# Performance work log

Measured on AMD Instinct MI355X. Metric: run time of the kernel, lower is better.

## Reference

```python
import jax, jax.numpy as jnp
import numpy as np

B, C_IN, N_PTS = 16, 4, 4096
N_P, DIM = 32, 256
EPS = 1e-5


def conv1d(x, w, b):
    # 1x1 Conv1d: x (B,C,N), w (O,C), b (O)
    return jnp.einsum('bcn,oc->bon', x, w) + b[None, :, None]


def bn(x, g, be):
    # BatchNorm1d in training mode: batch statistics over (B, N)
    m = jnp.mean(x, axis=(0, 2), keepdims=True)
    v = jnp.var(x, axis=(0, 2), keepdims=True)
    return g[None, :, None] * (x - m) * jax.lax.rsqrt(v + EPS) + be[None, :, None]


def softpool(x, n_p=N_P):
    # x: (B, C, N). For each sorting channel c, take indices of its top n_p
    # points and gather ALL C feature channels at those points.
    _, idx = jax.lax.top_k(x, n_p)            # (B, C_sort, n_p) indices into N
    g = jax.vmap(lambda xb, ib: xb[:, ib])(x, idx)  # (B, C_feat, C_sort, n_p)
    return jnp.transpose(g, (0, 1, 3, 2))     # (B, C_feat, n_p, C_sort)


def _forward(x, w1, b1, g1, be1, w2, b2, g2, be2, w3, b3, g3, be3,
             w8, b8, w9, b9, w4, b4, g4, be4, w5, b5, g5, be5,
             w6, b6, g6, be6, w7, b7):
    h = jax.nn.relu(bn(conv1d(x, w1, b1), g1, be1))      # (B,64,N)
    pointfeat = h
    h = jax.nn.relu(bn(conv1d(h, w2, b2), g2, be2))      # (B,128,N)
    h = bn(conv1d(h, w3, b3), g3, be3)                   # (B,256,N)
    sp = softpool(h)                                     # (B,256,32,256)
    # conv8: Conv2d(256,256,(1,256)) -> (B,256,32)
    y = jnp.einsum('bchw,ocw->boh', sp, w8) + b8[None, :, None]
    # conv9: Conv2d(256,256,(32,1)) -> (B,256)
    y = jnp.einsum('bch,och->bo', y, w9) + b9[None, :]
    glob = jnp.broadcast_to(y[:, :, None], (x.shape[0], DIM, x.shape[2]))
    h = jnp.concatenate([glob, pointfeat], axis=1)       # (B,320,N)
    h = jax.nn.relu(bn(conv1d(h, w4, b4), g4, be4))      # (B,512,N)
    h = jax.nn.relu(bn(conv1d(h, w5, b5), g5, be5))      # (B,256,N)
    h = jax.nn.relu(bn(conv1d(h, w6, b6), g6, be6))      # (B,128,N)
    return jnp.tanh(conv1d(h, w7, b7))                   # (B,3,N)


def setup_inputs() -> dict:
    key = jax.random.key(0)
    ks = iter(jax.random.split(key, 64))
    def p(shape, scale=0.05):
        return (jax.random.normal(next(ks), shape, jnp.float32) * scale)
    inp = {}
    inp['x'] = jax.random.normal(next(ks), (B, C_IN, N_PTS), jnp.float32)
    for name, o, i in [('1', 64, 4), ('2', 128, 64), ('3', 256, 128),
                       ('4', 512, 320), ('5', 256, 512), ('6', 128, 256)]:
        inp['w' + name] = p((o, i))
        inp['b' + name] = p((o,))
        inp['g' + name] = jnp.ones((o,), jnp.float32)
        inp['be' + name] = jnp.zeros((o,), jnp.float32)
    inp['w7'] = p((3, 128)); inp['b7'] = p((3,))
    inp['w8'] = p((DIM, DIM, DIM)); inp['b8'] = p((DIM,))
    inp['w9'] = p((DIM, DIM, N_P)); inp['b9'] = p((DIM,))
    return inp


def reference(x, w1, b1, g1, be1, w2, b2, g2, be2, w3, b3, g3, be3,
              w4, b4, g4, be4, w5, b5, g5, be5, w6, b6, g6, be6,
              w7, b7, w8, b8, w9, b9):
    return _forward(x, w1, b1, g1, be1, w2, b2, g2, be2, w3, b3, g3, be3,
                    w8, b8, w9, b9, w4, b4, g4, be4, w5, b5, g5, be5,
                    w6, b6, g6, be6, w7, b7)
```

## Files before the change

### kernel.cpp

```cpp
#include <hip/hip_runtime.h>
#include <cstdint>
#include <cstddef>

#define NPTS 4096
#define BATCH 16

typedef unsigned int uint32;
typedef unsigned short u16;

typedef __attribute__((ext_vector_type(8))) short short8;
typedef __attribute__((ext_vector_type(16))) float float16;

__device__ __forceinline__ u16 f2bf(float f) {
  uint32 u = __float_as_uint(f);
  u = (u + 0x7fffu + ((u >> 16) & 1u)) >> 16;
  return (u16)u;
}
__device__ __forceinline__ float bf2f(u16 h) {
  return __uint_as_float(((uint32)h) << 16);
}

__global__ __launch_bounds__(256) void conv_gemm(
    const float* __restrict__ act, const float* __restrict__ wt,
    const float* __restrict__ rowbias, const float* __restrict__ obias,
    const float* __restrict__ inScale, const float* __restrict__ inShift,
    float* __restrict__ out, float* __restrict__ partials, int C, int O)
{
  __shared__ float As[16][68];
  __shared__ float Ws[16][68];
  __shared__ float redS[64][17];
  __shared__ float redQ[64][17];
  const int b  = blockIdx.z;
  const int o0 = blockIdx.y * 64;
  const int n0 = blockIdx.x * 64;
  const int t  = threadIdx.x;
  const int tx = t & 15, ty = t >> 4;
  float acc[4][4] = {};
  const float* actb = act + ((size_t)b * C) * NPTS;

  for (int k0 = 0; k0 < C; k0 += 16) {
    const int r  = ty;
    const int cs = tx * 4;
    const int k  = k0 + r;
    float4 av = make_float4(0.f, 0.f, 0.f, 0.f);
    if (k < C) {
      av = *(const float4*)(actb + (size_t)k * NPTS + n0 + cs);
      if (inScale) {
        const float scv = inScale[k], shv = inShift[k];
        av.x = fmaxf(fmaf(av.x, scv, shv), 0.f);
        av.y = fmaxf(fmaf(av.y, scv, shv), 0.f);
        av.z = fmaxf(fmaf(av.z, scv, shv), 0.f);
        av.w = fmaxf(fmaf(av.w, scv, shv), 0.f);
      }
    }
    *(float4*)&As[r][cs] = av;

    float4 wv = make_float4(0.f, 0.f, 0.f, 0.f);
    if (k < C) {
      const float* wp = wt + (size_t)k * O;
      const int o = o0 + cs;
      if (o + 3 < O) {
        wv = *(const float4*)&wp[o];
      } else {
        float tmp[4] = {0.f, 0.f, 0.f, 0.f};
        for (int j = 0; j < 4; ++j) if (o + j < O) tmp[j] = wp[o + j];
        wv = make_float4(tmp[0], tmp[1], tmp[2], tmp[3]);
      }
    }
    *(float4*)&Ws[r][cs] = wv;
    __syncthreads();

    const int kmax = (C - k0 < 16) ? (C - k0) : 16;
    for (int kk = 0; kk < kmax; ++kk) {
      float4 a = *(float4*)&As[kk][tx * 4];
      float4 w = *(float4*)&Ws[kk][ty * 4];
      acc[0][0] += w.x * a.x; acc[0][1] += w.x * a.y; acc[0][2] += w.x * a.z; acc[0][3] += w.x * a.w;
      acc[1][0] += w.y * a.x; acc[1][1] += w.y * a.y; acc[1][2] += w.y * a.z; acc[1][3] += w.y * a.w;
      acc[2][0] += w.z * a.x; acc[2][1] += w.z * a.y; acc[2][2] += w.z * a.z; acc[2][3] += w.z * a.w;
      acc[3][0] += w.w * a.x; acc[3][1] += w.w * a.y; acc[3][2] += w.w * a.z; acc[3][3] += w.w * a.w;
    }
    __syncthreads();
  }

  float s[4], q[4];
  for (int i = 0; i < 4; ++i) {
    const int o = o0 + ty * 4 + i;
    s[i] = 0.f; q[i] = 0.f;
    if (o >= O) continue;
    float base = 0.f;
    if (rowbias) base  = rowbias[(size_t)b * O + o];
    if (obias)   base += obias[o];
    float4 v = make_float4(acc[i][0] + base, acc[i][1] + base, acc[i][2] + base, acc[i][3] + base);
    *(float4*)&out[((size_t)b * O + o) * NPTS + n0 + tx * 4] = v;
    s[i] = v.x + v.y + v.z + v.w;
    q[i] = v.x * v.x + v.y * v.y + v.z * v.z + v.w * v.w;
  }

  if (partials) {
    for (int i = 0; i < 4; ++i) { redS[ty * 4 + i][tx] = s[i]; redQ[ty * 4 + i][tx] = q[i]; }
    __syncthreads();
    if (t < 64) {
      float a = 0.f;
      for (int j = 0; j < 16; ++j) a += redS[t][j];
      partials[((size_t)b * O + o0 + t) * 64 + blockIdx.x] = a;
    } else if (t < 128) {
      float a = 0.f;
      for (int j = 0; j < 16; ++j) a += redQ[t - 64][j];
      partials[(size_t)BATCH * O * 64 + ((size_t)b * O + o0 + t - 64) * 64 + blockIdx.x] = a;
    }
  }
}

__global__ __launch_bounds__(256) void pack_wmfma(const float* __restrict__ src,
                                                  u16* __restrict__ ph, u16* __restrict__ pl,
                                                  int O, int Ctot, int cOff, int Csub) {
  int i = blockIdx.x * 256 + threadIdx.x;
  if (i >= O * Csub) return;
  const int KS = Csub >> 4;
  int j    = i & 7;
  int lj   = (i >> 3) & 63;
  int mtks = i >> 9;
  int ks   = mtks % KS;
  int mt   = mtks / KS;
  int o = mt * 32 + (lj & 31);
  int c = ks * 16 + (lj >> 5) * 8 + j;
  float v = src[(size_t)o * Ctot + cOff + c];
  u16 h = f2bf(v);
  ph[i] = h;
  pl[i] = f2bf(v - bf2f(h));
}

__global__ __launch_bounds__(256) void conv_mfma(
    const float* __restrict__ act, const u16* __restrict__ wh, const u16* __restrict__ wl,
    const float* __restrict__ rowbias,
    const float* __restrict__ inScale, const float* __restrict__ inShift,
    float* __restrict__ out, float* __restrict__ ps, int C, int O)
{
  __shared__ u16 Bh[4096];
  __shared__ u16 Bl[4096];
  const int b  = blockIdx.z;
  const int o0 = blockIdx.y * 128;
  const int n0 = blockIdx.x * 128;
  const int t  = threadIdx.x;
  const int l  = t & 63, wva = t >> 6;
  const int mt = blockIdx.y * 4 + wva;
  const int KS = C >> 4;
  const float* actb = act + ((size_t)b * C) * NPTS;

  float16 acc[4];
#pragma unroll
  for (int ns = 0; ns < 4; ++ns)
#pragma unroll
    for (int r = 0; r < 16; ++r) acc[ns][r] = 0.f;

  const int cq = t >> 5;
  const int nq = t & 31;
  const int nn = n0 + nq * 4;
  const int ksl = cq >> 2, oct = (cq >> 1) & 1, j0 = (cq & 1) * 4;

  for (int k0 = 0; k0 < C; k0 += 32) {
    const int cb = k0 + cq * 4;
    float va[4][4];
#pragma unroll
    for (int i2 = 0; i2 < 4; ++i2) {
      float4 v4 = *(const float4*)(actb + (size_t)(cb + i2) * NPTS + nn);
      if (inScale) {
        const float scv = inScale[cb + i2], shv = inShift[cb + i2];
        v4.x = fmaxf(fmaf(v4.x, scv, shv), 0.f);
        v4.y = fmaxf(fmaf(v4.y, scv, shv), 0.f);
        v4.z = fmaxf(fmaf(v4.z, scv, shv), 0.f);
        v4.w = fmaxf(fmaf(v4.w, scv, shv), 0.f);
      }
      va[i2][0] = v4.x; va[i2][1] = v4.y; va[i2][2] = v4.z; va[i2][3] = v4.w;
    }
    const size_t abase = (((size_t)mt * KS + (k0 >> 4)) * 64 + l) * 8;
    short8 AH0 = *(const short8*)(wh + abase);
    short8 AH1 = *(const short8*)(wh + abase + 512);
    short8 AL0 = *(const short8*)(wl + abase);
    short8 AL1 = *(const short8*)(wl + abase + 512);

    __syncthreads();
#pragma unroll
    for (int d = 0; d < 4; ++d) {
      const int nrel = nq * 4 + d;
      const int ns = nrel >> 5, li = nrel & 31;
      u16 h0 = f2bf(va[0][d]), h1 = f2bf(va[1][d]), h2 = f2bf(va[2][d]), h3 = f2bf(va[3][d]);
      u16 q0 = f2bf(va[0][d] - bf2f(h0));
      u16 q1 = f2bf(va[1][d] - bf2f(h1));
      u16 q2 = f2bf(va[2][d] - bf2f(h2));
      u16 q3 = f2bf(va[3][d] - bf2f(h3));
      const int idx = ((ksl * 4 + ns) * 64 + oct * 32 + li) * 8 + j0;
      *(ushort4*)&Bh[idx] = make_ushort4(h0, h1, h2, h3);
      *(ushort4*)&Bl[idx] = make_ushort4(q0, q1, q2, q3);
    }
    __syncthreads();

#pragma unroll
    for (int ns = 0; ns < 4; ++ns) {
      short8 BH0 = *(const short8*)&Bh[((0 * 4 + ns) * 64 + l) * 8];
      short8 BL0 = *(const short8*)&Bl[((0 * 4 + ns) * 64 + l) * 8];
      acc[ns] = __builtin_amdgcn_mfma_f32_32x32x16_bf16(AH0, BH0, acc[ns], 0, 0, 0);
      acc[ns] = __builtin_amdgcn_mfma_f32_32x32x16_bf16(AL0, BH0, acc[ns], 0, 0, 0);
      acc[ns] = __builtin_amdgcn_mfma_f32_32x32x16_bf16(AH0, BL0, acc[ns], 0, 0, 0);
      short8 BH1 = *(const short8*)&Bh[((1 * 4 + ns) * 64 + l) * 8];
      short8 BL1 = *(const short8*)&Bl[((1 * 4 + ns) * 64 + l) * 8];
      acc[ns] = __builtin_amdgcn_mfma_f32_32x32x16_bf16(AH1, BH1, acc[ns], 0, 0, 0);
      acc[ns] = __builtin_amdgcn_mfma_f32_32x32x16_bf16(AL1, BH1, acc[ns], 0, 0, 0);
      acc[ns] = __builtin_amdgcn_mfma_f32_32x32x16_bf16(AH1, BL1, acc[ns], 0, 0, 0);
    }
  }

  const int col = l & 31, half = l >> 5;
  float sv[16], sq[16];
#pragma unroll
  for (int r = 0; r < 16; ++r) {
    const int o = o0 + wva * 32 + (r & 3) + 8 * (r >> 2) + 4 * half;
    const float base = rowbias ? rowbias[(size_t)b * O + o] : 0.f;
    float s = 0.f, q = 0.f;
#pragma unroll
    for (int ns = 0; ns < 4; ++ns) {
      float val = acc[ns][r] + base;
      out[((size_t)b * O + o) * NPTS + n0 + ns * 32 + col] = val;
      s += val; q += val * val;
    }
    sv[r] = s; sq[r] = q;
  }
  if (ps) {
#pragma unroll
    for (int r = 0; r < 16; ++r) {
#pragma unroll
      for (int m = 1; m < 32; m <<= 1) {
        sv[r] += __shfl_xor(sv[r], m, 64);
        sq[r] += __shfl_xor(sq[r], m, 64);
      }
    }
    if (col == 0) {
#pragma unroll
      for (int r = 0; r < 16; ++r) {
        const int o = o0 + wva * 32 + (r & 3) + 8 * (r >> 2) + 4 * half;
        ps[((size_t)b * O + o) * 32 + blockIdx.x] = sv[r];
        ps[(size_t)BATCH * O * 32 + ((size_t)b * O + o) * 32 + blockIdx.x] = sq[r];
      }
    }
  }
}

__global__ __launch_bounds__(256) void bn_finalize(const float* __restrict__ ps,
                                                   const float* __restrict__ g, const float* __restrict__ be,
                                                   float* __restrict__ scale, float* __restrict__ shift,
                                                   int O, int NT) {
  const int c = blockIdx.x;
  const int total = BATCH * NT;
  const float* p2 = ps + (size_t)BATCH * O * NT;
  const int t = threadIdx.x;
  float s = 0.f, q = 0.f;
  for (int e = t; e < total; e += 256) {
    const int b = e / NT, nt = e - b * NT;
    const size_t a = ((size_t)b * O + c) * NT + nt;
    s += ps[a];
    q += p2[a];
  }
#pragma unroll
  for (int m = 32; m; m >>= 1) {
    s += __shfl_down(s, m, 64);
    q += __shfl_down(q, m, 64);
  }
  __shared__ float lsS[4], lsQ[4];
  const int wid = t >> 6;
  if ((t & 63) == 0) { lsS[wid] = s; lsQ[wid] = q; }
  __syncthreads();
  if (t == 0) {
    s = lsS[0] + lsS[1] + lsS[2] + lsS[3];
    q = lsQ[0] + lsQ[1] + lsQ[2] + lsQ[3];
    const float inv = 1.f / 65536.f;
    float m   = s * inv;
    float var = q * inv - m * m;
    float sc  = g[c] * rsqrtf(var + 1e-5f);
    scale[c] = sc;
    shift[c] = be[c] - m * sc;
  }
}

__global__ __launch_bounds__(256) void topk_kernel(const float* __restrict__ h3,
                                                   int* __restrict__ idxp) {
  __shared__ float wvv[4];
  __shared__ int   wvi[4];
  __shared__ int   bcI;
  const int c = blockIdx.x, b = blockIdx.y;
  const float* src = h3 + ((size_t)b * 256 + c) * NPTS;
  const int t = threadIdx.x;
  float v[16];
  float bv = -INFINITY; int bi = NPTS;
#pragma unroll
  for (int s = 0; s < 16; ++s) {
    v[s] = src[t + 256 * s];
    if (v[s] > bv) { bv = v[s]; bi = t + 256 * s; }
  }
  int* dst = idxp + ((size_t)b * 256 + c) * 32;
  for (int r = 0; r < 32; ++r) {
    float rv = bv; int ri = bi;
#pragma unroll
    for (int off = 32; off; off >>= 1) {
      float ov = __shfl_down(rv, off, 64);
      int   oi = __shfl_down(ri, off, 64);
      if (ov > rv || (ov == rv && oi < ri)) { rv = ov; ri = oi; }
    }
    if ((t & 63) == 0) { wvv[t >> 6] = rv; wvi[t >> 6] = ri; }
    __syncthreads();
    if (t == 0) {
      for (int k = 1; k < 4; ++k)
        if (wvv[k] > rv || (wvv[k] == rv && wvi[k] < ri)) { rv = wvv[k]; ri = wvi[k]; }
      dst[r] = ri;
      bcI = ri;
    }
    __syncthreads();
    const int wi_ = bcI;
    if ((wi_ & 255) == t) {
      const int slot = wi_ >> 8;
#pragma unroll
      for (int s = 0; s < 16; ++s) if (s == slot) v[s] = -INFINITY;
      bv = -INFINITY; bi = NPTS;
#pragma unroll
      for (int s = 0; s < 16; ++s) if (v[s] > bv) { bv = v[s]; bi = t + 256 * s; }
    }
  }
}

__global__ __launch_bounds__(256) void transpose_h3(const float* __restrict__ h3,
                                                    float* __restrict__ h3T,
                                                    const float* __restrict__ sc,
                                                    const float* __restrict__ sh) {
  __shared__ float tile[32][33];
  const int b = blockIdx.z;
  const int n0 = blockIdx.x * 32, c0 = blockIdx.y * 32;
  const int tx = threadIdx.x & 31, ty = threadIdx.x >> 5;
  const float* src = h3 + (size_t)b * 256 * NPTS;
  for (int j = 0; j < 4; ++j)
    tile[ty + j * 8][tx] = src[(size_t)(c0 + ty + j * 8) * NPTS + n0 + tx];
  __syncthreads();
  float* dst = h3T + (size_t)b * NPTS * 256;
  const float scv = sc[c0 + tx], shv = sh[c0 + tx];
  for (int j = 0; j < 4; ++j)
    dst[(size_t)(n0 + ty + j * 8) * 256 + c0 + tx] = fmaf(tile[tx][ty + j * 8], scv, shv);
}

__global__ __launch_bounds__(256) void transpose_w8(const float* __restrict__ w8,
                                                    float* __restrict__ w8t) {
  __shared__ float tile[64][65];
  const int m0 = blockIdx.x * 64, w0 = blockIdx.y * 64;
  const int tx = threadIdx.x & 63, ty = threadIdx.x >> 6;
  for (int j = 0; j < 16; ++j)
    tile[ty + j * 4][tx] = w8[(size_t)(m0 + ty + j * 4) * 256 + w0 + tx];
  __syncthreads();
  for (int j = 0; j < 16; ++j)
    w8t[(size_t)(w0 + ty + j * 4) * 65536 + m0 + tx] = tile[tx][ty + j * 4];
}

__global__ __launch_bounds__(256) void pack_w8(const float* __restrict__ w8t,
                                               u16* __restrict__ w8h, u16* __restrict__ w8l) {
  size_t i = (size_t)blockIdx.x * 256 + threadIdx.x;
  int j  = (int)(i & 7);
  int lj = (int)((i >> 3) & 63);
  int ks = (int)((i >> 9) & 15);
  int mt = (int)((i >> 13) & 7);
  int w  = (int)(i >> 16);
  int o  = mt * 32 + (lj & 31);
  int c  = ks * 16 + (lj >> 5) * 8 + j;
  float v = w8t[((size_t)w << 16) + (size_t)o * 256 + c];
  u16 h = f2bf(v);
  w8h[i] = h;
  w8l[i] = f2bf(v - bf2f(h));
}

#define Y8N (BATCH * 256 * 32)
__global__ __launch_bounds__(256, 1) void conv8_mfma(
    const float* __restrict__ h3T, const u16* __restrict__ w8h,
    const u16* __restrict__ w8l, const int* __restrict__ idxp,
    float* __restrict__ y8p)
{
  __shared__ u16 G[2][8192];
  const int wg = blockIdx.x;
  const int oq = blockIdx.y;
  const int bg = blockIdx.z;
  const int t  = threadIdx.x;
  const int l  = t & 63, wv = t >> 6;
  const int mt = oq * 4 + wv;

  float16 accH[4], accL[4];
  for (int i = 0; i < 4; ++i)
    for (int r = 0; r < 16; ++r) { accH[i][r] = 0.f; accL[i][r] = 0.f; }

  short8 ah[16], al[16];
  const int hrow  = t >> 3;
  const int cbase = (t & 7) * 32;
  float4 g4[8];

  auto issueG = [&](int step) {
    int wi = step >> 2, bi = step & 3;
    int w = wg * 8 + wi;
    int b = bg * 4 + bi;
    int n = idxp[((size_t)b * 256 + w) * 32 + hrow];
    const float* src = h3T + ((size_t)b * NPTS + n) * 256 + cbase;
#pragma unroll
    for (int j = 0; j < 8; ++j) g4[j] = *(const float4*)&src[j * 4];
  };
  auto writeG = [&](int buf) {
#pragma unroll
    for (int a = 0; a < 4; ++a) {
      int c8 = (cbase >> 3) + a;
      int ks = c8 >> 1;
      int lp = hrow + (c8 & 1) * 32;
      float4 v0 = g4[a * 2], v1 = g4[a * 2 + 1];
      uint32 u0 = (uint32)f2bf(v0.x) | ((uint32)f2bf(v0.y) << 16);
      uint32 u1 = (uint32)f2bf(v0.z) | ((uint32)f2bf(v0.w) << 16);
      uint32 u2 = (uint32)f2bf(v1.x) | ((uint32)f2bf(v1.y) << 16);
      uint32 u3 = (uint32)f2bf(v1.z) | ((uint32)f2bf(v1.w) << 16);
      *(uint4*)&G[buf][((size_t)ks * 64 + lp) * 8] = make_uint4(u0, u1, u2, u3);
    }
  };

  issueG(0); writeG(0);
  __syncthreads();

  for (int wi = 0; wi < 8; ++wi) {
    const int w = wg * 8 + wi;
    {
      const size_t base = (((size_t)w * 8 + mt) * 16) * 512 + (size_t)l * 8;
#pragma unroll
      for (int ks = 0; ks < 16; ++ks) {
        ah[ks] = *(const short8*)(w8h + base + ks * 512);
        al[ks] = *(const short8*)(w8l + base + ks * 512);
      }
    }
#pragma unroll
    for (int bi = 0; bi < 4; ++bi) {
      const int step = wi * 4 + bi;
      const int cur = bi & 1;
      if (step < 31) issueG(step + 1);
      const u16* Gc = G[cur];
#pragma unroll
      for (int ks = 0; ks < 16; ++ks) {
        short8 bf = *(const short8*)&Gc[((size_t)ks * 64 + l) * 8];
        accH[bi] = __builtin_amdgcn_mfma_f32_32x32x16_bf16(ah[ks], bf, accH[bi], 0, 0, 0);
        accL[bi] = __builtin_amdgcn_mfma_f32_32x32x16_bf16(al[ks], bf, accL[bi], 0, 0, 0);
      }
      if (step < 31) writeG(1 - cur);
      __syncthreads();
    }
  }

  const int h = l & 31;
  const int rbase = oq * 128 + wv * 32 + 4 * (l >> 5);
#pragma unroll
  for (int bi = 0; bi < 4; ++bi) {
    int b = bg * 4 + bi;
    float* dst = y8p + ((size_t)(wg * BATCH + b) * 256) * 32;
#pragma unroll
    for (int r = 0; r < 16; ++r) {
      int o = rbase + (r & 3) + 8 * (r >> 2);
      dst[(size_t)o * 32 + h] = accH[bi][r] + accL[bi][r];
    }
  }
}

__global__ __launch_bounds__(256) void y8_reduce(const float* __restrict__ y8p,
                                                 const float* __restrict__ b8,
                                                 float* __restrict__ y8) {
  int i = blockIdx.x * 256 + threadIdx.x;
  float s = b8[(i >> 5) & 255];
#pragma unroll
  for (int p = 0; p < 32; ++p) s += y8p[(size_t)p * Y8N + i];
  y8[i] = s;
}

__global__ __launch_bounds__(256) void conv9_kernel(const float* __restrict__ y8,
                                                    const float* __restrict__ w9,
                                                    const float* __restrict__ b9,
                                                    float* __restrict__ y9) {
  const int o = blockIdx.x, b = blockIdx.y;
  const float* yb = y8 + (size_t)b * 8192;
  const float* wo = w9 + (size_t)o * 8192;
  float s = 0.f;
  for (int i = threadIdx.x * 4; i < 8192; i += 1024) {
    float4 v = *(const float4*)&yb[i];
    float4 u = *(const float4*)&wo[i];
    s += v.x * u.x + v.y * u.y + v.z * u.z + v.w * u.w;
  }
  for (int off = 32; off; off >>= 1) s += __shfl_down(s, off, 64);
  __shared__ float ls[4];
  const int wid = threadIdx.x >> 6;
  if ((threadIdx.x & 63) == 0) ls[wid] = s;
  __syncthreads();
  if (threadIdx.x == 0) y9[(size_t)b * 256 + o] = ls[0] + ls[1] + ls[2] + ls[3] + b9[o];
}

__global__ __launch_bounds__(256) void cvec_kernel(const float* __restrict__ y9,
                                                   const float* __restrict__ w4,
                                                   float* __restrict__ cvec) {
  int tid = blockIdx.x * 256 + threadIdx.x;
  if (tid >= BATCH * 512) return;
  const int b = tid >> 9, o = tid & 511;
  const float* row = w4 + (size_t)o * 320;
  const float* yb  = y9 + (size_t)b * 256;
  float s = 0.f;
  for (int c = 0; c < 256; c += 4) {
    float4 u = *(const float4*)&row[c];
    s += u.x * yb[c] + u.y * yb[c + 1] + u.z * yb[c + 2] + u.w * yb[c + 3];
  }
  cvec[(size_t)b * 512 + o] = s;
}

__global__ __launch_bounds__(256) void transpose_w(const float* __restrict__ src,
                                                   float* __restrict__ dst,
                                                   int O, int Ctot, int cOff, int Csub) {
  int i = blockIdx.x * 256 + threadIdx.x;
  if (i >= O * Csub) return;
  int c = i / O, o = i - c * O;
  dst[(size_t)c * O + o] = src[(size_t)o * Ctot + cOff + c];
}

__global__ __launch_bounds__(256) void tanh_out(const float* __restrict__ raw,
                                                float* __restrict__ out) {
  int i = blockIdx.x * 256 + threadIdx.x;
  if (i < BATCH * 3 * NPTS) out[i] = tanhf(raw[i]);
}

extern "C" void kernel_launch(void* const* d_in, const int* in_sizes, int n_in,
                              void* d_out, int out_size, void* d_ws, size_t ws_size,
                              hipStream_t stream) {
  (void)in_sizes; (void)n_in; (void)ws_size; (void)out_size;
  const float* x   = (const float*)d_in[0];
  const float* w1  = (const float*)d_in[1];
  const float* g1  = (const float*)d_in[3];
  const float* be1 = (const float*)d_in[4];
  const float* w2  = (const float*)d_in[5];
  const float* g2  = (const float*)d_in[7];
  const float* be2 = (const float*)d_in[8];
  const float* w3  = (const float*)d_in[9];
  const float* g3  = (const float*)d_in[11];
  const float* be3 = (const float*)d_in[12];
  const float* w4  = (const float*)d_in[13];
  const float* g4  = (const float*)d_in[15];
  const float* be4 = (const float*)d_in[16];
  const float* w5  = (const float*)d_in[17];
  const float* g5  = (const float*)d_in[19];
  const float* be5 = (const float*)d_in[20];
  const float* w6  = (const float*)d_in[21];
  const float* g6  = (const float*)d_in[23];
  const float* be6 = (const float*)d_in[24];
  const float* w7  = (const float*)d_in[25];
  const float* b7  = (const float*)d_in[26];
  const float* w8  = (const float*)d_in[27];
  const float* b8  = (const float*)d_in[28];
  const float* w9  = (const float*)d_in[29];
  const float* b9  = (const float*)d_in[30];

  char* ws = (char*)d_ws;
  size_t off = 0;
  auto alloc = [&](size_t bytes) -> void* {
    void* p = ws + off;
    off += (bytes + 255) & ~(size_t)255;
    return p;
  };
  float* Q1  = (float*)alloc((size_t)BATCH * 64  * NPTS * 4);
  float* Q2  = (float*)alloc((size_t)BATCH * 128 * NPTS * 4);
  float* Q3  = (float*)alloc((size_t)BATCH * 256 * NPTS * 4);
  float* Q4  = (float*)alloc((size_t)BATCH * 256 * NPTS * 4);
  float* Q5  = (float*)alloc((size_t)BATCH * 256 * NPTS * 4);
  int*   idx  = (int*)alloc((size_t)BATCH * 256 * 32 * 4);
  float* y8   = (float*)alloc((size_t)Y8N * 4);
  float* y9   = (float*)alloc((size_t)BATCH * 256 * 4);
  float* cvec = (float*)alloc((size_t)BATCH * 512 * 4);
  float* ps   = (float*)alloc((size_t)2 * BATCH * 512 * 64 * 4);
  float* scb  = (float*)alloc((size_t)6 * 1024 * 4);
  float* w1t  = (float*)alloc(4   * 64  * 4);
  float* w2t  = (float*)alloc(64  * 128 * 4);
  float* w3t  = (float*)alloc(128 * 256 * 4);
  float* w7t  = (float*)alloc(128 * 3   * 4);
  u16* ph4 = (u16*)alloc(512 * 64  * 2);  u16* pl4 = (u16*)alloc(512 * 64  * 2);
  u16* ph5 = (u16*)alloc(256 * 512 * 2);  u16* pl5 = (u16*)alloc(256 * 512 * 2);
  u16* ph6 = (u16*)alloc(128 * 256 * 2);  u16* pl6 = (u16*)alloc(128 * 256 * 2);

  float* w8t = Q4;
  u16*   w8h = (u16*)Q5;
  u16*   w8l = (u16*)Q5 + (size_t)16777216;
  float* y8p = Q2;
  float* h4  = Q2;

  float* sc[6]; float* sh[6];
  for (int i = 0; i < 6; ++i) { sc[i] = scb + i * 1024; sh[i] = scb + i * 1024 + 512; }

  transpose_w<<<(4 * 64 + 255) / 256,   256, 0, stream>>>(w1, w1t, 64, 4, 0, 4);
  transpose_w<<<(64 * 128 + 255) / 256, 256, 0, stream>>>(w2, w2t, 128, 64, 0, 64);
  transpose_w<<<(128 * 256 + 255) / 256,256, 0, stream>>>(w3, w3t, 256, 128, 0, 128);
  transpose_w<<<(128 * 3 + 255) / 256,  256, 0, stream>>>(w7, w7t, 3, 128, 0, 128);
  pack_wmfma<<<(512 * 64  + 255) / 256, 256, 0, stream>>>(w4, ph4, pl4, 512, 320, 256, 64);
  pack_wmfma<<<(256 * 512 + 255) / 256, 256, 0, stream>>>(w5, ph5, pl5, 256, 512, 0,   512);
  pack_wmfma<<<(128 * 256 + 255) / 256, 256, 0, stream>>>(w6, ph6, pl6, 128, 256, 0,   256);
  transpose_w8<<<dim3(1024, 4), 256, 0, stream>>>(w8, w8t);
  pack_w8<<<65536, 256, 0, stream>>>(w8t, w8h, w8l);

  conv_gemm<<<dim3(64, 1, BATCH), 256, 0, stream>>>(x, w1t, nullptr, nullptr, nullptr, nullptr, Q1, ps, 4, 64);
  bn_finalize<<<64, 256, 0, stream>>>(ps, g1, be1, sc[0], sh[0], 64, 64);
  conv_gemm<<<dim3(64, 2, BATCH), 256, 0, stream>>>(Q1, w2t, nullptr, nullptr, sc[0], sh[0], Q2, ps, 64, 128);
  bn_finalize<<<128, 256, 0, stream>>>(ps, g2, be2, sc[1], sh[1], 128, 64);
  conv_gemm<<<dim3(64, 4, BATCH), 256, 0, stream>>>(Q2, w3t, nullptr, nullptr, sc[1], sh[1], Q3, ps, 128, 256);
  bn_finalize<<<256, 256, 0, stream>>>(ps, g3, be3, sc[2], sh[2], 256, 64);

  topk_kernel<<<dim3(256, BATCH), 256, 0, stream>>>(Q3, idx);
  transpose_h3<<<dim3(NPTS / 32, 8, BATCH), 256, 0, stream>>>(Q3, Q4, sc[2], sh[2]);

  conv8_mfma<<<dim3(32, 2, 4), 256, 0, stream>>>(Q4, w8h, w8l, idx, y8p);
  y8_reduce<<<Y8N / 256, 256, 0, stream>>>(y8p, b8, y8);
  conv9_kernel<<<dim3(256, BATCH), 256, 0, stream>>>(y8, w9, b9, y9);
  cvec_kernel<<<(BATCH * 512 + 255) / 256, 256, 0, stream>>>(y9, w4, cvec);

  conv_mfma<<<dim3(32, 4, BATCH), 256, 0, stream>>>(Q1, ph4, pl4, cvec, sc[0], sh[0], h4, ps, 64, 512);
  bn_finalize<<<512, 256, 0, stream>>>(ps, g4, be4, sc[3], sh[3], 512, 32);
  conv_mfma<<<dim3(32, 2, BATCH), 256, 0, stream>>>(h4, ph5, pl5, nullptr, sc[3], sh[3], Q5, ps, 512, 256);
  bn_finalize<<<256, 256, 0, stream>>>(ps, g5, be5, sc[4], sh[4], 256, 32);
  conv_mfma<<<dim3(32, 1, BATCH), 256, 0, stream>>>(Q5, ph6, pl6, nullptr, sc[4], sh[4], Q2, ps, 256, 128);
  bn_finalize<<<128, 256, 0, stream>>>(ps, g6, be6, sc[5], sh[5], 128, 32);
  conv_gemm<<<dim3(64, 1, BATCH), 256, 0, stream>>>(Q2, w7t, nullptr, b7, sc[5], sh[5], Q1, nullptr, 128, 3);
  tanh_out<<<(BATCH * 3 * NPTS) / 256, 256, 0, stream>>>(Q1, (float*)d_out);
}
```

Measured before the change: 783.6 us.

## Double-buffer conv_mfma LDS tiles and fuse w8 transpose with bf16 packing

conv_mfma now uses two LDS buffers, so global loads of the next K-chunk are issued before the MFMAs on the current chunk. The BN scale/shift, bf16 conversion and LDS writes for that next chunk happen after the MFMAs, which leaves one barrier per iteration instead of two. Separately, the w8 transpose and split-bf16 packing are fused into one kernel, removing an intermediate 256MB fp32 write and read. The cost is double the LDS and more live registers, which may reduce occupancy.

Measured after the change: 763.6 us. 2.5% less time.

```diff
diff --git a/kernel.cpp b/kernel.cpp
--- a/kernel.cpp
+++ b/kernel.cpp
@@ -136,8 +136,8 @@
     const float* __restrict__ inScale, const float* __restrict__ inShift,
     float* __restrict__ out, float* __restrict__ ps, int C, int O)
 {
-  __shared__ u16 Bh[4096];
-  __shared__ u16 Bl[4096];
+  __shared__ u16 Bh[2][4096];
+  __shared__ u16 Bl[2][4096];
   const int b  = blockIdx.z;
   const int o0 = blockIdx.y * 128;
   const int n0 = blockIdx.x * 128;
@@ -145,6 +145,7 @@
   const int l  = t & 63, wva = t >> 6;
   const int mt = blockIdx.y * 4 + wva;
   const int KS = C >> 4;
+  const int NCH = C >> 5;
   const float* actb = act + ((size_t)b * C) * NPTS;
 
   float16 acc[4];
@@ -158,28 +159,32 @@
   const int nn = n0 + nq * 4;
   const int ksl = cq >> 2, oct = (cq >> 1) & 1, j0 = (cq & 1) * 4;
 
-  for (int k0 = 0; k0 < C; k0 += 32) {
-    const int cb = k0 + cq * 4;
-    float va[4][4];
+  float va[4][4];
+  float4 scv = make_float4(1.f,1.f,1.f,1.f), shv = make_float4(0.f,0.f,0.f,0.f);
+
+  auto loadChunk = [&](int ch) {
+    const int cb = ch * 32 + cq * 4;
 #pragma unroll
     for (int i2 = 0; i2 < 4; ++i2) {
       float4 v4 = *(const float4*)(actb + (size_t)(cb + i2) * NPTS + nn);
-      if (inScale) {
-        const float scv = inScale[cb + i2], shv = inShift[cb + i2];
-        v4.x = fmaxf(fmaf(v4.x, scv, shv), 0.f);
-        v4.y = fmaxf(fmaf(v4.y, scv, shv), 0.f);
-        v4.z = fmaxf(fmaf(v4.z, scv, shv), 0.f);
-        v4.w = fmaxf(fmaf(v4.w, scv, shv), 0.f);
-      }
       va[i2][0] = v4.x; va[i2][1] = v4.y; va[i2][2] = v4.z; va[i2][3] = v4.w;
     }
-    const size_t abase = (((size_t)mt * KS + (k0 >> 4)) * 64 + l) * 8;
-    short8 AH0 = *(const short8*)(wh + abase);
-    short8 AH1 = *(const short8*)(wh + abase + 512);
-    short8 AL0 = *(const short8*)(wl + abase);
-    short8 AL1 = *(const short8*)(wl + abase + 512);
-
-    __syncthreads();
+    if (inScale) {
+      scv = *(const float4*)&inScale[cb];
+      shv = *(const float4*)&inShift[cb];
+    }
+  };
+  auto applyBN = [&]() {
+    if (!inScale) return;
+#pragma unroll
+    for (int d = 0; d < 4; ++d) {
+      va[0][d] = fmaxf(fmaf(va[0][d], scv.x, shv.x), 0.f);
+      va[1][d] = fmaxf(fmaf(va[1][d], scv.y, shv.y), 0.f);
+      va[2][d] = fmaxf(fmaf(va[2][d], scv.z, shv.z), 0.f);
+      va[3][d] = fmaxf(fmaf(va[3][d], scv.w, shv.w), 0.f);
+    }
+  };
+  auto convWrite = [&](int buf) {
 #pragma unroll
     for (int d = 0; d < 4; ++d) {
       const int nrel = nq * 4 + d;
@@ -190,24 +195,42 @@
       u16 q2 = f2bf(va[2][d] - bf2f(h2));
       u16 q3 = f2bf(va[3][d] - bf2f(h3));
       const int idx = ((ksl * 4 + ns) * 64 + oct * 32 + li) * 8 + j0;
-      *(ushort4*)&Bh[idx] = make_ushort4(h0, h1, h2, h3);
-      *(ushort4*)&Bl[idx] = make_ushort4(q0, q1, q2, q3);
-    }
-    __syncthreads();
-
+      *(ushort4*)&Bh[buf][idx] = make_ushort4(h0, h1, h2, h3);
+      *(ushort4*)&Bl[buf][idx] = make_ushort4(q0, q1, q2, q3);
+    }
+  };
+
+  loadChunk(0);
+  applyBN();
+  convWrite(0);
+  __syncthreads();
+
+  for (int ch = 0; ch < NCH; ++ch) {
+    const size_t abase = (((size_t)mt * KS + ch * 2) * 64 + (size_t)l) * 8;
+    short8 AH0 = *(const short8*)(wh + abase);
+    short8 AH1 = *(const short8*)(wh + abase + 512);
+    short8 AL0 = *(const short8*)(wl + abase);
+    short8 AL1 = *(const short8*)(wl + abase + 512);
+    const bool more = (ch + 1 < NCH);
+    if (more) loadChunk(ch + 1);
+
+    const u16* bh = Bh[ch & 1];
+    const u16* bl = Bl[ch & 1];
 #pragma unroll
     for (int ns = 0; ns < 4; ++ns) {
-      short8 BH0 = *(const short8*)&Bh[((0 * 4 + ns) * 64 + l) * 8];
-      short8 BL0 = *(const short8*)&Bl[((0 * 4 + ns) * 64 + l) * 8];
-      acc[ns] = __builtin_amdgcn_mfma_f32_32x32x16_bf16(AH0, BH0, acc[ns], 0, 0, 0);
+      short8 BH0 = *(const short8*)&bh[((0 * 4 + ns) * 64 + l) * 8];
+      short8 BL0 = *(const short8*)&bl[((0 * 4 + ns) * 64 + l) * 8];
       acc[ns] = __builtin_amdgcn_mfma_f32_32x32x16_bf16(AL0, BH0, acc[ns], 0, 0, 0);
       acc[ns] = __builtin_amdgcn_mfma_f32_32x32x16_bf16(AH0, BL0, acc[ns], 0, 0, 0);
-      short8 BH1 = *(const short8*)&Bh[((1 * 4 + ns) * 64 + l) * 8];
-      short8 BL1 = *(const short8*)&Bl[((1 * 4 + ns) * 64 + l) * 8];
-      acc[ns] = __builtin_amdgcn_mfma_f32_32x32x16_bf16(AH1, BH1, acc[ns], 0, 0, 0);
+      acc[ns] = __builtin_amdgcn_mfma_f32_32x32x16_bf16(AH0, BH0, acc[ns], 0, 0, 0);
+      short8 BH1 = *(const short8*)&bh[((4 + ns) * 64 + l) * 8];
+      short8 BL1 = *(const short8*)&bl[((4 + ns) * 64 + l) * 8];
       acc[ns] = __builtin_amdgcn_mfma_f32_32x32x16_bf16(AL1, BH1, acc[ns], 0, 0, 0);
       acc[ns] = __builtin_amdgcn_mfma_f32_32x32x16_bf16(AH1, BL1, acc[ns], 0, 0, 0);
-    }
+      acc[ns] = __builtin_amdgcn_mfma_f32_32x32x16_bf16(AH1, BH1, acc[ns], 0, 0, 0);
+    }
+    if (more) { applyBN(); convWrite((ch + 1) & 1); }
+    __syncthreads();
   }
 
   const int col = l & 31, half = l >> 5;
@@ -344,32 +367,30 @@
     dst[(size_t)(n0 + ty + j * 8) * 256 + c0 + tx] = fmaf(tile[tx][ty + j * 8], scv, shv);
 }
 
-__global__ __launch_bounds__(256) void transpose_w8(const float* __restrict__ w8,
-                                                    float* __restrict__ w8t) {
+__global__ __launch_bounds__(256) void transpack_w8(const float* __restrict__ w8,
+                                                    u16* __restrict__ w8h, u16* __restrict__ w8l) {
   __shared__ float tile[64][65];
   const int m0 = blockIdx.x * 64, w0 = blockIdx.y * 64;
   const int tx = threadIdx.x & 63, ty = threadIdx.x >> 6;
+#pragma unroll
   for (int j = 0; j < 16; ++j)
     tile[ty + j * 4][tx] = w8[(size_t)(m0 + ty + j * 4) * 256 + w0 + tx];
   __syncthreads();
-  for (int j = 0; j < 16; ++j)
-    w8t[(size_t)(w0 + ty + j * 4) * 65536 + m0 + tx] = tile[tx][ty + j * 4];
-}
-
-__global__ __launch_bounds__(256) void pack_w8(const float* __restrict__ w8t,
-                                               u16* __restrict__ w8h, u16* __restrict__ w8l) {
-  size_t i = (size_t)blockIdx.x * 256 + threadIdx.x;
-  int j  = (int)(i & 7);
-  int lj = (int)((i >> 3) & 63);
-  int ks = (int)((i >> 9) & 15);
-  int mt = (int)((i >> 13) & 7);
-  int w  = (int)(i >> 16);
-  int o  = mt * 32 + (lj & 31);
-  int c  = ks * 16 + (lj >> 5) * 8 + j;
-  float v = w8t[((size_t)w << 16) + (size_t)o * 256 + c];
-  u16 h = f2bf(v);
-  w8h[i] = h;
-  w8l[i] = f2bf(v - bf2f(h));
+  const int m = m0 + tx;
+  const int o = m >> 8, c = m & 255;
+  const int mt = (o >> 5) & 7;
+  const int lane = (o & 31) + ((c >> 3) & 1) * 32;
+  const int ks = (c >> 4) & 15;
+  const int jj = c & 7;
+#pragma unroll
+  for (int j = 0; j < 16; ++j) {
+    const int w = w0 + ty + j * 4;
+    float v = tile[tx][ty + j * 4];
+    size_t f = ((((size_t)w * 8 + mt) * 16 + ks) * 64 + lane) * 8 + jj;
+    u16 h = f2bf(v);
+    w8h[f] = h;
+    w8l[f] = f2bf(v - bf2f(h));
+  }
 }
 
 #define Y8N (BATCH * 256 * 32)
@@ -581,7 +602,6 @@
   u16* ph5 = (u16*)alloc(256 * 512 * 2);  u16* pl5 = (u16*)alloc(256 * 512 * 2);
   u16* ph6 = (u16*)alloc(128 * 256 * 2);  u16* pl6 = (u16*)alloc(128 * 256 * 2);
 
-  float* w8t = Q4;
   u16*   w8h = (u16*)Q5;
   u16*   w8l = (u16*)Q5 + (size_t)16777216;
   float* y8p = Q2;
@@ -597,8 +617,7 @@
   pack_wmfma<<<(512 * 64  + 255) / 256, 256, 0, stream>>>(w4, ph4, pl4, 512, 320, 256, 64);
   pack_wmfma<<<(256 * 512 + 255) / 256, 256, 0, stream>>>(w5, ph5, pl5, 256, 512, 0,   512);
   pack_wmfma<<<(128 * 256 + 255) / 256, 256, 0, stream>>>(w6, ph6, pl6, 128, 256, 0,   256);
-  transpose_w8<<<dim3(1024, 4), 256, 0, stream>>>(w8, w8t);
-  pack_w8<<<65536, 256, 0, stream>>>(w8t, w8h, w8l);
+  transpack_w8<<<dim3(1024, 4), 256, 0, stream>>>(w8, w8h, w8l);
 
   conv_gemm<<<dim3(64, 1, BATCH), 256, 0, stream>>>(x, w1t, nullptr, nullptr, nullptr, nullptr, Q1, ps, 4, 64);
   bn_finalize<<<64, 256, 0, stream>>>(ps, g1, be1, sc[0], sh[0], 64, 64);
```
